# Kernel tuning notes

Hardware: AMD Instinct MI355X
Metric: run time of the kernel (lower is better)

The kernel has to match this reference:

```python
import jax, jax.numpy as jnp
import numpy as np

B, N, A = 32, 1024, 256          # batch, n_entities, n_agents
D_IN, D_H, H = 256, 256, 8       # input_dim, hidden_dim, n_heads
SCALE = 1.0 / np.sqrt(D_H)
EPS = 1e-12


def setup_inputs() -> dict:
    key = jax.random.key(0)
    ks = jax.random.split(key, 7)
    x = jax.random.normal(ks[0], (B, N, D_IN), dtype=jnp.float32)
    # binary visibility mask [batch, n_agents, n_entities]
    m = (jax.random.uniform(ks[1], (B, A, N)) > 0.5).astype(jnp.float32)
    # encoder Linear(input_dim, hidden_dim): weight [out,in], bias [out]
    W_enc = jax.random.normal(ks[2], (D_H, D_IN), dtype=jnp.float32) / np.sqrt(D_IN)
    b_enc = jnp.zeros((D_H,), dtype=jnp.float32)
    # per-head projection matrices stacked [H, D_H, D_H] (torch.randn init)
    WQ = jax.random.normal(ks[3], (H, D_H, D_H), dtype=jnp.float32)
    WK = jax.random.normal(ks[4], (H, D_H, D_H), dtype=jnp.float32)
    WV = jax.random.normal(ks[5], (H, D_H, D_H), dtype=jnp.float32)
    return {"x": x, "m": m, "W_enc": W_enc, "b_enc": b_enc, "WQ": WQ, "WK": WK, "WV": WV}


def reference(x, m, W_enc, b_enc, WQ, WK, WV):
    # encode: LeakyReLU then Linear
    h = jnp.einsum('bni,oi->bno', jax.nn.leaky_relu(x), W_enc) + b_enc  # [B,N,D_H]
    n_agents = m.shape[1]
    ha = h[:, :n_agents]                                   # [B,A,D_H]
    # per-head projections, heads vectorized
    Q = jnp.einsum('bad,hde->bhae', ha, WQ)                # [B,H,A,D_H]
    K = jnp.einsum('bnd,hde->bhne', h, WK)                 # [B,H,N,D_H]
    V = jnp.einsum('bnd,hde->bhne', h, WV)                 # [B,H,N,D_H]
    S = jnp.einsum('bhae,bhne->bhan', Q, K) * SCALE        # [B,H,A,N]
    P = jax.nn.softmax(S, axis=-1)
    P = P * m[:, None]                                     # post-softmax mask
    prob = P / (jnp.sum(P, axis=-1, keepdims=True) + EPS)  # renormalize
    z = jnp.einsum('bhan,bhne->bhae', prob, V)             # [B,H,A,D_H]
    return jnp.mean(z, axis=1)                             # [B,A,D_H]
```

## Files before the change

kernel.cpp:

```cpp
#include <hip/hip_runtime.h>
#include <math.h>

namespace {
constexpr int B_N  = 32;
constexpr int SEQ  = 1024;
constexpr int AG   = 256;
constexpr int D    = 256;
constexpr int NH   = 8;
constexpr float SCALE = 0.0625f;
constexpr float EPS   = 1e-12f;

constexpr size_t HHI_OFF  = 0;
constexpr size_t HLO_OFF  = 16777216;
constexpr size_t HT_OFF   = 33554432;
constexpr size_t MTHI_OFF = 50331648;
constexpr size_t MTLO_OFF = 51380224;
constexpr size_t MB_OFF   = 52428800;
constexpr size_t WVT_OFF  = 53477376;
constexpr size_t Z16_OFF  = 54525952;
}

typedef __attribute__((ext_vector_type(8))) short short8;
typedef __attribute__((ext_vector_type(4))) float floatx4;
#define MFMA_BF(A,B,C) __builtin_amdgcn_mfma_f32_16x16x32_bf16(A,B,C,0,0,0)

__device__ __forceinline__ unsigned short bf16_rtne(float f) {
    unsigned u = __float_as_uint(f);
    u += 0x7fffu + ((u >> 16) & 1u);
    return (unsigned short)(u >> 16);
}
__device__ __forceinline__ float bf16_tof(unsigned short h) {
    return __uint_as_float(((unsigned)h) << 16);
}
__device__ __forceinline__ void async16(void* lds, const void* g) {
    __builtin_amdgcn_global_load_lds(
        (const __attribute__((address_space(1))) unsigned int*)g,
        (__attribute__((address_space(3))) unsigned int*)lds,
        16, 0, 0);
}

__global__ __launch_bounds__(256) void enc_mfma(
    const float* __restrict__ x, const float* __restrict__ W_enc,
    const float* __restrict__ b_enc,
    ushort* __restrict__ h_hi, ushort* __restrict__ h_lo,
    ushort* __restrict__ hT)
{
    __shared__ ushort Ah[64][40], Al[64][40];
    __shared__ ushort Bh[64][40], Bl[64][40];
    __shared__ ushort Th[64][72], Tl[64][72];

    const int t    = threadIdx.x;
    const int wv   = t >> 6;
    const int lane = t & 63;
    const int l15  = lane & 15;
    const int quad = lane >> 4;
    const int col0 = blockIdx.x * 64;
    const int row0 = blockIdx.y * 64;

    floatx4 acc[4];
#pragma unroll
    for (int i = 0; i < 4; ++i) acc[i] = (floatx4){0.f, 0.f, 0.f, 0.f};

    for (int k0 = 0; k0 < 256; k0 += 32) {
        __syncthreads();
        {
            const int r = t >> 2, s = (t & 3) * 8;
            float f[8];
            *(float4*)&f[0] = *(const float4*)(x + (size_t)(row0 + r) * 256 + k0 + s);
            *(float4*)&f[4] = *(const float4*)(x + (size_t)(row0 + r) * 256 + k0 + s + 4);
            short8 hi8, lo8;
#pragma unroll
            for (int e = 0; e < 8; ++e) {
                float v = f[e] > 0.f ? f[e] : 0.01f * f[e];
                unsigned short hb = bf16_rtne(v);
                hi8[e] = (short)hb;
                lo8[e] = (short)bf16_rtne(v - bf16_tof(hb));
            }
            *(short8*)&Ah[r][s] = hi8;
            *(short8*)&Al[r][s] = lo8;
            *(float4*)&f[0] = *(const float4*)(W_enc + (size_t)(col0 + r) * 256 + k0 + s);
            *(float4*)&f[4] = *(const float4*)(W_enc + (size_t)(col0 + r) * 256 + k0 + s + 4);
#pragma unroll
            for (int e = 0; e < 8; ++e) {
                unsigned short hb = bf16_rtne(f[e]);
                hi8[e] = (short)hb;
                lo8[e] = (short)bf16_rtne(f[e] - bf16_tof(hb));
            }
            *(short8*)&Bh[r][s] = hi8;
            *(short8*)&Bl[r][s] = lo8;
        }
        __syncthreads();

        short8 Af  = *(const short8*)&Ah[wv * 16 + l15][quad * 8];
        short8 Afl = *(const short8*)&Al[wv * 16 + l15][quad * 8];
#pragma unroll
        for (int et = 0; et < 4; ++et) {
            short8 Bf  = *(const short8*)&Bh[et * 16 + l15][quad * 8];
            short8 Bfl = *(const short8*)&Bl[et * 16 + l15][quad * 8];
            acc[et] = MFMA_BF(Af,  Bf,  acc[et]);
            acc[et] = MFMA_BF(Afl, Bf,  acc[et]);
            acc[et] = MFMA_BF(Af,  Bfl, acc[et]);
        }
    }

    __syncthreads();
#pragma unroll
    for (int et = 0; et < 4; ++et) {
        const int col = et * 16 + l15;
        const float bb = b_enc[col0 + col];
#pragma unroll
        for (int r = 0; r < 4; ++r) {
            const int row = wv * 16 + quad * 4 + r;
            const float v = acc[et][r] + bb;
            const unsigned short hb = bf16_rtne(v);
            Th[row][col] = hb;
            Tl[row][col] = bf16_rtne(v - bf16_tof(hb));
        }
    }
    __syncthreads();
    {
        const int r = t >> 2, c0 = (t & 3) * 16;
        ushort* dh = h_hi + (size_t)(row0 + r) * 256 + col0 + c0;
        ushort* dl = h_lo + (size_t)(row0 + r) * 256 + col0 + c0;
        *(short8*)dh       = *(const short8*)&Th[r][c0];
        *(short8*)(dh + 8) = *(const short8*)&Th[r][c0 + 8];
        *(short8*)dl       = *(const short8*)&Tl[r][c0];
        *(short8*)(dl + 8) = *(const short8*)&Tl[r][c0 + 8];
    }
    {
        const int bq = (int)blockIdx.y >> 4;
        const int n0 = ((int)blockIdx.y & 15) * 64;
        const int dd = t >> 2, seg = (t & 3) * 16;
        ushort tmp[16];
#pragma unroll
        for (int j = 0; j < 16; ++j) tmp[j] = Th[seg + j][dd];
        ushort* dst = hT + ((size_t)(bq * 256 + col0 + dd)) * 1024 + n0 + seg;
        *(short8*)dst       = *(short8*)&tmp[0];
        *(short8*)(dst + 8) = *(short8*)&tmp[8];
    }
}

__global__ __launch_bounds__(256) void prep_fused(
    const float* __restrict__ m, unsigned* __restrict__ mb,
    const float* __restrict__ WV, ushort* __restrict__ WVt,
    const float* __restrict__ WQ, const float* __restrict__ WK,
    ushort* __restrict__ Mt_hi, ushort* __restrict__ Mt_lo)
{
    __shared__ __align__(16) char plds[17408];
    const int t = threadIdx.x;
    const int v = blockIdx.x;

    if (v < 1024) {
        const int idx = v * 256 + t;
        const float4* src = (const float4*)(m + (size_t)idx * 32);
        unsigned wbits = 0;
#pragma unroll
        for (int i = 0; i < 8; ++i) {
            float4 vv = src[i];
            wbits |= (vv.x > 0.5f ? 1u : 0u) << (i * 4 + 0);
            wbits |= (vv.y > 0.5f ? 1u : 0u) << (i * 4 + 1);
            wbits |= (vv.z > 0.5f ? 1u : 0u) << (i * 4 + 2);
            wbits |= (vv.w > 0.5f ? 1u : 0u) << (i * 4 + 3);
        }
        mb[idx] = wbits;
    } else if (v < 1152) {
        float (*T)[68] = (float(*)[68])plds;
        const int v2 = v - 1024;
        const int d0 = (v2 & 3) * 64, e0 = ((v2 >> 2) & 3) * 64, h = v2 >> 4;
        {
            const int r = t >> 2, c = (t & 3) * 16;
            const float* src = WV + ((size_t)(h * 256 + d0 + r)) * 256 + e0 + c;
#pragma unroll
            for (int j = 0; j < 4; ++j)
                *(float4*)&T[r][c + j * 4] = *(const float4*)(src + j * 4);
        }
        __syncthreads();
        {
            const int ee = t >> 2, seg = (t & 3) * 16;
            ushort tmp[16];
#pragma unroll
            for (int j = 0; j < 16; ++j) tmp[j] = bf16_rtne(T[seg + j][ee]);
            ushort* dst = WVt + ((size_t)(h * 256 + e0 + ee)) * 256 + d0 + seg;
            *(short8*)dst       = *(short8*)&tmp[0];
            *(short8*)(dst + 8) = *(short8*)&tmp[8];
        }
    } else {
        float (*AsT)[68] = (float(*)[68])plds;
        float (*BsT)[68] = (float(*)[68])(plds + 8704);
        const int v3 = v - 1152;
        const int tx = t & 15, ty = t >> 4;
        const int col0 = (v3 & 3) * 64;
        const int row0 = ((v3 >> 2) & 3) * 64;
        const int hz   = v3 >> 4;
        const float* A  = WK + (size_t)hz * 256 * 256;
        const float* Bm = WQ + (size_t)hz * 256 * 256;
        ushort* Chi = Mt_hi + (size_t)hz * 256 * 256;
        ushort* Clo = Mt_lo + (size_t)hz * 256 * 256;

        float acc[4][4];
#pragma unroll
        for (int r = 0; r < 4; ++r)
#pragma unroll
            for (int c = 0; c < 4; ++c) acc[r][c] = 0.f;

        for (int k0 = 0; k0 < 256; k0 += 32) {
            __syncthreads();
#pragma unroll
            for (int ss = 0; ss < 2; ++ss) {
                int flat = t + 256 * ss;
                int rr = flat >> 3, k4 = flat & 7;
                float4 vv = *(const float4*)(A + (size_t)(row0 + rr) * 256 + k0 + k4 * 4);
                AsT[k4*4+0][rr] = vv.x; AsT[k4*4+1][rr] = vv.y;
                AsT[k4*4+2][rr] = vv.z; AsT[k4*4+3][rr] = vv.w;
                float4 wv = *(const float4*)(Bm + (size_t)(col0 + rr) * 256 + k0 + k4 * 4);
                BsT[k4*4+0][rr] = wv.x; BsT[k4*4+1][rr] = wv.y;
                BsT[k4*4+2][rr] = wv.z; BsT[k4*4+3][rr] = wv.w;
            }
            __syncthreads();
#pragma unroll 8
            for (int kk = 0; kk < 32; ++kk) {
                float4 a4 = *(const float4*)&AsT[kk][ty * 4];
                float4 b4 = *(const float4*)&BsT[kk][tx * 4];
                const float ar[4] = {a4.x, a4.y, a4.z, a4.w};
                const float bc[4] = {b4.x, b4.y, b4.z, b4.w};
#pragma unroll
                for (int r = 0; r < 4; ++r)
#pragma unroll
                    for (int c = 0; c < 4; ++c)
                        acc[r][c] = fmaf(ar[r], bc[c], acc[r][c]);
            }
        }
#pragma unroll
        for (int r = 0; r < 4; ++r) {
            const int row = row0 + ty * 4 + r;
            ushort hi4[4], lo4[4];
#pragma unroll
            for (int c = 0; c < 4; ++c) {
                float vv = acc[r][c];
                hi4[c] = bf16_rtne(vv);
                lo4[c] = bf16_rtne(vv - bf16_tof(hi4[c]));
            }
            *(ushort4*)(Chi + (size_t)row * 256 + col0 + tx * 4) =
                make_ushort4(hi4[0], hi4[1], hi4[2], hi4[3]);
            *(ushort4*)(Clo + (size_t)row * 256 + col0 + tx * 4) =
                make_ushort4(lo4[0], lo4[1], lo4[2], lo4[3]);
        }
    }
}

__global__ __launch_bounds__(512, 2) void attn_mfma(
    const ushort* __restrict__ h_hi, const ushort* __restrict__ h_lo,
    const ushort* __restrict__ hT,   const ushort* __restrict__ Mt_hi,
    const ushort* __restrict__ Mt_lo, const unsigned* __restrict__ mbits,
    ushort* __restrict__ zout)
{
    __shared__ __align__(16) char lds[118784];
    ushort* pP = (ushort*)(lds + 98304);
    ushort* pE = (ushort*)(lds + 108544);

    const int t    = threadIdx.x;
    const int wv   = t >> 6;
    const int lane = t & 63;
    const int l15  = lane & 15;
    const int quad = lane >> 4;
    const int f    = blockIdx.x;
    const int b    = (f & 7) + 8 * (f >> 7);
    const int mid  = (f >> 3) & 15;
    const int hh   = (mid >> 2) * 2 + (wv >> 2);
    const int a0   = (mid & 3) * 64;
    const int aw   = a0 + (wv & 3) * 16;

    const ushort* hbh = h_hi + (size_t)b * SEQ * D;
    const ushort* hbl = h_lo + (size_t)b * SEQ * D;
    const ushort* hTb = hT   + (size_t)b * D * SEQ;

    floatx4 qac[16];
#pragma unroll
    for (int i = 0; i < 16; ++i) qac[i] = (floatx4){0.f, 0.f, 0.f, 0.f};

    for (int kc = 0; kc < 4; ++kc) {
        short8 Ah[2], Al[2];
#pragma unroll
        for (int kt = 0; kt < 2; ++kt) {
            const size_t ao = ((size_t)b * SEQ + aw + l15) * D +
                              kc * 64 + kt * 32 + quad * 8;
            Ah[kt] = *(const short8*)(h_hi + ao);
            Al[kt] = *(const short8*)(h_lo + ao);
        }
#pragma unroll
        for (int nt2 = 0; nt2 < 16; ++nt2) {
#pragma unroll
            for (int kt = 0; kt < 2; ++kt) {
                const size_t mo = ((size_t)hh * D + nt2 * 16 + l15) * D +
                                  kc * 64 + kt * 32 + quad * 8;
                short8 Bh = *(const short8*)(Mt_hi + mo);
                short8 Bl = *(const short8*)(Mt_lo + mo);
                qac[nt2] = MFMA_BF(Ah[kt], Bh, qac[nt2]);
                qac[nt2] = MFMA_BF(Al[kt], Bh, qac[nt2]);
                qac[nt2] = MFMA_BF(Ah[kt], Bl, qac[nt2]);
            }
        }
    }

    short8 Qhi[8], Qlo[8];
    {
        float* qscr = (float*)lds;
        for (int c = 0; c < 4; ++c) {
#pragma unroll
            for (int j = 0; j < 4; ++j)
#pragma unroll
                for (int r = 0; r < 4; ++r)
                    qscr[(wv * 16 + quad * 4 + r) * 68 + j * 16 + l15] = qac[c * 4 + j][r];
#pragma unroll
            for (int kt = 0; kt < 2; ++kt) {
                const float* pr = &qscr[(wv * 16 + l15) * 68 + kt * 32 + quad * 8];
                float ftmp[8];
                *(float4*)&ftmp[0] = *(const float4*)pr;
                *(float4*)&ftmp[4] = *(const float4*)(pr + 4);
                short8 hi, lo;
#pragma unroll
                for (int e = 0; e < 8; ++e) {
                    unsigned short hb = bf16_rtne(ftmp[e]);
                    hi[e] = (short)hb;
                    lo[e] = (short)bf16_rtne(ftmp[e] - bf16_tof(hb));
                }
                Qhi[c * 2 + kt] = hi;
                Qlo[c * 2 + kt] = lo;
            }
        }
    }
    __syncthreads();

    auto issue_tile = [&](char* buf, int n0) {
        ushort* dh = (ushort*)buf;
        ushort* dl = (ushort*)(buf + 16384);
        ushort* dT = (ushort*)(buf + 32768);
#pragma unroll
        for (int i = 0; i < 2; ++i) {
            const int slot = wv * 128 + i * 64 + lane;
            const int row  = slot >> 5;
            const int p    = slot & 31;
            const int c    = p ^ (row & 7);
            const size_t go = (size_t)(n0 + row) * 256 + c * 8;
            const size_t lo_ = (size_t)(wv * 128 + i * 64) * 8;
            async16(dh + lo_, hbh + go);
            async16(dl + lo_, hbl + go);
        }
#pragma unroll
        for (int i = 0; i < 2; ++i) {
            const int slot = wv * 128 + i * 64 + lane;
            const int row  = slot >> 2;
            const int p    = slot & 3;
            const int c    = p ^ ((row >> 2) & 3);
            async16(dT + (size_t)(wv * 128 + i * 64) * 8,
                    hTb + (size_t)row * 1024 + n0 + c * 8);
        }
    };

    issue_tile(lds,         0);
    issue_tile(lds + 49152, 32);
    __syncthreads();

    floatx4 zac[16];
#pragma unroll
    for (int i = 0; i < 16; ++i) zac[i] = (floatx4){0.f, 0.f, 0.f, 0.f};
    floatx4 zacZ = (floatx4){0.f, 0.f, 0.f, 0.f};
    floatx4 zacE = (floatx4){0.f, 0.f, 0.f, 0.f};
    float mx[4] = {-INFINITY, -INFINITY, -INFINITY, -INFINITY};

    short8 onesf;
#pragma unroll
    for (int e = 0; e < 8; ++e) onesf[e] = (short)0x3F80;

    const unsigned* mbr = mbits + ((size_t)b * AG + aw + quad * 4) * (SEQ / 32);

    for (int nt = 0; nt < 32; ++nt) {
        char* cur = lds + (size_t)(nt & 1) * 49152;
        ushort* hS_hi = (ushort*)cur;
        ushort* hS_lo = (ushort*)(cur + 16384);
        ushort* hTS   = (ushort*)(cur + 32768);

        floatx4 sacH[2], sacL[2];
        sacH[0] = (floatx4){0.f, 0.f, 0.f, 0.f};
        sacH[1] = (floatx4){0.f, 0.f, 0.f, 0.f};
        sacL[0] = (floatx4){0.f, 0.f, 0.f, 0.f};
        sacL[1] = (floatx4){0.f, 0.f, 0.f, 0.f};
#pragma unroll
        for (int ks = 0; ks < 8; ++ks) {
            const int cg = ks * 4 + quad;
#pragma unroll
            for (int ntile = 0; ntile < 2; ++ntile) {
                const int row = ntile * 16 + l15;
                const int off = row * 256 + (cg ^ (row & 7)) * 8;
                short8 Bh = *(const short8*)&hS_hi[off];
                short8 Bl = *(const short8*)&hS_lo[off];
                sacH[ntile] = MFMA_BF(Qhi[ks], Bh, sacH[ntile]);
                sacL[ntile] = MFMA_BF(Qlo[ks], Bh, sacL[ntile]);
                sacL[ntile] = MFMA_BF(Qhi[ks], Bl, sacL[ntile]);
            }
        }

        float l0[4], l1[4];
#pragma unroll
        for (int r = 0; r < 4; ++r) {
            l0[r] = (sacH[0][r] + sacL[0][r]) * SCALE;
            l1[r] = (sacH[1][r] + sacL[1][r]) * SCALE;
        }

        float mt[4];
#pragma unroll
        for (int r = 0; r < 4; ++r) mt[r] = fmaxf(l0[r], l1[r]);
#pragma unroll
        for (int off = 1; off < 16; off <<= 1) {
#pragma unroll
            for (int r = 0; r < 4; ++r)
                mt[r] = fmaxf(mt[r], __shfl_xor(mt[r], off));
        }

        const bool need = (mt[0] > mx[0] + 8.0f) || (mt[1] > mx[1] + 8.0f) ||
                          (mt[2] > mx[2] + 8.0f) || (mt[3] > mx[3] + 8.0f);
        if (__any(need)) {
            float alr[4];
#pragma unroll
            for (int r = 0; r < 4; ++r) {
                const float mxn = fmaxf(mx[r], mt[r]);
                alr[r] = __expf(mx[r] - mxn);
                mx[r] = mxn;
            }
#pragma unroll
            for (int dt = 0; dt < 16; ++dt) {
                zac[dt][0] *= alr[0]; zac[dt][1] *= alr[1];
                zac[dt][2] *= alr[2]; zac[dt][3] *= alr[3];
            }
            zacZ[0] *= alr[0]; zacZ[1] *= alr[1];
            zacZ[2] *= alr[2]; zacZ[3] *= alr[3];
            zacE[0] *= alr[0]; zacE[1] *= alr[1];
            zacE[2] *= alr[2]; zacE[3] *= alr[3];
        }

#pragma unroll
        for (int r = 0; r < 4; ++r) {
            const unsigned w0 = mbr[r * (SEQ / 32) + nt];
            const float e0 = __expf(l0[r] - mx[r]);
            const float e1 = __expf(l1[r] - mx[r]);
            const float p0 = ((w0 >> l15) & 1u)        ? e0 : 0.f;
            const float p1 = ((w0 >> (16 + l15)) & 1u) ? e1 : 0.f;
            const int row = wv * 16 + quad * 4 + r;
            pP[row * 40 + l15]      = bf16_rtne(p0);
            pP[row * 40 + 16 + l15] = bf16_rtne(p1);
            pE[row * 40 + l15]      = bf16_rtne(e0);
            pE[row * 40 + 16 + l15] = bf16_rtne(e1);
        }

        short8 Pf = *(const short8*)&pP[(wv * 16 + l15) * 40 + quad * 8];
        short8 Ef = *(const short8*)&pE[(wv * 16 + l15) * 40 + quad * 8];
        zacZ = MFMA_BF(Pf, onesf, zacZ);
        zacE = MFMA_BF(Ef, onesf, zacE);

#pragma unroll
        for (int dt = 0; dt < 16; ++dt) {
            const int row = dt * 16 + l15;
            const int p   = quad ^ ((row >> 2) & 3);
            short8 Bf = *(const short8*)&hTS[row * 32 + p * 8];
            zac[dt] = MFMA_BF(Pf, Bf, zac[dt]);
        }

        __syncthreads();
        if (nt + 2 < 32) issue_tile(cur, (nt + 2) * 32);
    }

#pragma unroll
    for (int r = 0; r < 4; ++r) {
        const int a = aw + quad * 4 + r;
        const float inv = 1.0f / (zacZ[r] + EPS * zacE[r]);
        ushort* zr = zout + (((size_t)b * NH + hh) * AG + a) * D;
#pragma unroll
        for (int dt = 0; dt < 16; ++dt)
            zr[dt * 16 + l15] = bf16_rtne(zac[dt][r] * inv);
    }
}

__global__ __launch_bounds__(256) void out_mfma(
    const ushort* __restrict__ z16, const ushort* __restrict__ WVt,
    float* __restrict__ out)
{
    const int t    = threadIdx.x;
    const int wv   = t >> 6;
    const int lane = t & 63;
    const int l15  = lane & 15;
    const int quad = lane >> 4;
    const int f    = blockIdx.x;
    const int b    = (f & 7) + 8 * (f >> 7);
    const int mid  = (f >> 3) & 15;
    const int e0   = (mid & 3) * 64;
    const int a0   = (mid >> 2) * 64;
    const int aw   = a0 + wv * 16;

    floatx4 acc[4];
#pragma unroll
    for (int i = 0; i < 4; ++i) acc[i] = (floatx4){0.f, 0.f, 0.f, 0.f};

#pragma unroll 4
    for (int c = 0; c < 64; ++c) {
        const int hh = c >> 3, d0 = (c & 7) * 32;
        short8 Af = *(const short8*)(z16 +
            (((size_t)b * NH + hh) * AG + aw + l15) * D + d0 + quad * 8);
#pragma unroll
        for (int et = 0; et < 4; ++et) {
            short8 Bf = *(const short8*)(WVt +
                ((size_t)hh * D + e0 + et * 16 + l15) * D + d0 + quad * 8);
            acc[et] = MFMA_BF(Af, Bf, acc[et]);
        }
    }
#pragma unroll
    for (int et = 0; et < 4; ++et)
#pragma unroll
        for (int r = 0; r < 4; ++r)
            out[((size_t)b * AG + aw + quad * 4 + r) * D + e0 + et * 16 + l15] =
                acc[et][r] * 0.125f;
}

extern "C" void kernel_launch(void* const* d_in, const int* in_sizes, int n_in,
                              void* d_out, int out_size, void* d_ws, size_t ws_size,
                              hipStream_t stream)
{
    (void)in_sizes; (void)n_in; (void)out_size; (void)ws_size;
    const float* x     = (const float*)d_in[0];
    const float* m     = (const float*)d_in[1];
    const float* W_enc = (const float*)d_in[2];
    const float* b_enc = (const float*)d_in[3];
    const float* WQ    = (const float*)d_in[4];
    const float* WK    = (const float*)d_in[5];
    const float* WV    = (const float*)d_in[6];
    float* out = (float*)d_out;
    char* ws = (char*)d_ws;

    ushort*   h_hi  = (ushort*)(ws + HHI_OFF);
    ushort*   h_lo  = (ushort*)(ws + HLO_OFF);
    ushort*   hT    = (ushort*)(ws + HT_OFF);
    ushort*   Mt_hi = (ushort*)(ws + MTHI_OFF);
    ushort*   Mt_lo = (ushort*)(ws + MTLO_OFF);
    unsigned* mbits = (unsigned*)(ws + MB_OFF);
    ushort*   WVt   = (ushort*)(ws + WVT_OFF);
    ushort*   z16   = (ushort*)(ws + Z16_OFF);

    enc_mfma<<<dim3(4, 512, 1), dim3(256), 0, stream>>>(
        x, W_enc, b_enc, h_hi, h_lo, hT);
    prep_fused<<<dim3(1280, 1, 1), dim3(256), 0, stream>>>(
        m, mbits, WV, WVt, WQ, WK, Mt_hi, Mt_lo);
    attn_mfma<<<dim3(512, 1, 1), dim3(512), 0, stream>>>(
        h_hi, h_lo, hT, Mt_hi, Mt_lo, mbits, z16);
    out_mfma<<<dim3(512, 1, 1), dim3(256), 0, stream>>>(z16, WVt, out);
}
```

Baseline: 527.3 us.

## Merge encoder and prep kernels into one launch; raise wave priority around MFMA loops

The encoder GEMM kernel and the mask/weight prep kernel are combined into a single launch of 3328 blocks, with blockIdx ranges dispatching to each role. This removes one kernel launch and the gap between the two, and lets the independent prep work overlap with the encoder work. s_setprio hints are also placed around the MFMA loops in the attention kernel so waves issuing matrix ops get scheduling priority. The shared LDS allocation grows to the encoder's size for every block, which may lower occupancy for the prep blocks.

```diff
diff --git a/kernel.cpp b/kernel.cpp
--- a/kernel.cpp
+++ b/kernel.cpp
@@ -39,119 +39,119 @@
         16, 0, 0);
 }
 
-__global__ __launch_bounds__(256) void enc_mfma(
+__global__ __launch_bounds__(256) void enc_prep(
     const float* __restrict__ x, const float* __restrict__ W_enc,
     const float* __restrict__ b_enc,
     ushort* __restrict__ h_hi, ushort* __restrict__ h_lo,
-    ushort* __restrict__ hT)
-{
-    __shared__ ushort Ah[64][40], Al[64][40];
-    __shared__ ushort Bh[64][40], Bl[64][40];
-    __shared__ ushort Th[64][72], Tl[64][72];
-
-    const int t    = threadIdx.x;
-    const int wv   = t >> 6;
-    const int lane = t & 63;
-    const int l15  = lane & 15;
-    const int quad = lane >> 4;
-    const int col0 = blockIdx.x * 64;
-    const int row0 = blockIdx.y * 64;
-
-    floatx4 acc[4];
-#pragma unroll
-    for (int i = 0; i < 4; ++i) acc[i] = (floatx4){0.f, 0.f, 0.f, 0.f};
-
-    for (int k0 = 0; k0 < 256; k0 += 32) {
-        __syncthreads();
-        {
-            const int r = t >> 2, s = (t & 3) * 8;
-            float f[8];
-            *(float4*)&f[0] = *(const float4*)(x + (size_t)(row0 + r) * 256 + k0 + s);
-            *(float4*)&f[4] = *(const float4*)(x + (size_t)(row0 + r) * 256 + k0 + s + 4);
-            short8 hi8, lo8;
-#pragma unroll
-            for (int e = 0; e < 8; ++e) {
-                float v = f[e] > 0.f ? f[e] : 0.01f * f[e];
-                unsigned short hb = bf16_rtne(v);
-                hi8[e] = (short)hb;
-                lo8[e] = (short)bf16_rtne(v - bf16_tof(hb));
-            }
-            *(short8*)&Ah[r][s] = hi8;
-            *(short8*)&Al[r][s] = lo8;
-            *(float4*)&f[0] = *(const float4*)(W_enc + (size_t)(col0 + r) * 256 + k0 + s);
-            *(float4*)&f[4] = *(const float4*)(W_enc + (size_t)(col0 + r) * 256 + k0 + s + 4);
-#pragma unroll
-            for (int e = 0; e < 8; ++e) {
-                unsigned short hb = bf16_rtne(f[e]);
-                hi8[e] = (short)hb;
-                lo8[e] = (short)bf16_rtne(f[e] - bf16_tof(hb));
-            }
-            *(short8*)&Bh[r][s] = hi8;
-            *(short8*)&Bl[r][s] = lo8;
-        }
-        __syncthreads();
-
-        short8 Af  = *(const short8*)&Ah[wv * 16 + l15][quad * 8];
-        short8 Afl = *(const short8*)&Al[wv * 16 + l15][quad * 8];
-#pragma unroll
-        for (int et = 0; et < 4; ++et) {
-            short8 Bf  = *(const short8*)&Bh[et * 16 + l15][quad * 8];
-            short8 Bfl = *(const short8*)&Bl[et * 16 + l15][quad * 8];
-            acc[et] = MFMA_BF(Af,  Bf,  acc[et]);
-            acc[et] = MFMA_BF(Afl, Bf,  acc[et]);
-            acc[et] = MFMA_BF(Af,  Bfl, acc[et]);
-        }
-    }
-
-    __syncthreads();
-#pragma unroll
-    for (int et = 0; et < 4; ++et) {
-        const int col = et * 16 + l15;
-        const float bb = b_enc[col0 + col];
-#pragma unroll
-        for (int r = 0; r < 4; ++r) {
-            const int row = wv * 16 + quad * 4 + r;
-            const float v = acc[et][r] + bb;
-            const unsigned short hb = bf16_rtne(v);
-            Th[row][col] = hb;
-            Tl[row][col] = bf16_rtne(v - bf16_tof(hb));
-        }
-    }
-    __syncthreads();
-    {
-        const int r = t >> 2, c0 = (t & 3) * 16;
-        ushort* dh = h_hi + (size_t)(row0 + r) * 256 + col0 + c0;
-        ushort* dl = h_lo + (size_t)(row0 + r) * 256 + col0 + c0;
-        *(short8*)dh       = *(const short8*)&Th[r][c0];
-        *(short8*)(dh + 8) = *(const short8*)&Th[r][c0 + 8];
-        *(short8*)dl       = *(const short8*)&Tl[r][c0];
-        *(short8*)(dl + 8) = *(const short8*)&Tl[r][c0 + 8];
-    }
-    {
-        const int bq = (int)blockIdx.y >> 4;
-        const int n0 = ((int)blockIdx.y & 15) * 64;
-        const int dd = t >> 2, seg = (t & 3) * 16;
-        ushort tmp[16];
-#pragma unroll
-        for (int j = 0; j < 16; ++j) tmp[j] = Th[seg + j][dd];
-        ushort* dst = hT + ((size_t)(bq * 256 + col0 + dd)) * 1024 + n0 + seg;
-        *(short8*)dst       = *(short8*)&tmp[0];
-        *(short8*)(dst + 8) = *(short8*)&tmp[8];
-    }
-}
-
-__global__ __launch_bounds__(256) void prep_fused(
+    ushort* __restrict__ hT,
     const float* __restrict__ m, unsigned* __restrict__ mb,
     const float* __restrict__ WV, ushort* __restrict__ WVt,
     const float* __restrict__ WQ, const float* __restrict__ WK,
     ushort* __restrict__ Mt_hi, ushort* __restrict__ Mt_lo)
 {
-    __shared__ __align__(16) char plds[17408];
+    __shared__ __align__(16) char slds[38912];
     const int t = threadIdx.x;
     const int v = blockIdx.x;
 
-    if (v < 1024) {
-        const int idx = v * 256 + t;
+    if (v < 2048) {
+        ushort (*Ah)[40] = (ushort(*)[40])(slds);
+        ushort (*Al)[40] = (ushort(*)[40])(slds + 5120);
+        ushort (*Bh)[40] = (ushort(*)[40])(slds + 10240);
+        ushort (*Bl)[40] = (ushort(*)[40])(slds + 15360);
+        ushort (*Th)[72] = (ushort(*)[72])(slds + 20480);
+        ushort (*Tl)[72] = (ushort(*)[72])(slds + 29696);
+
+        const int wv   = t >> 6;
+        const int lane = t & 63;
+        const int l15  = lane & 15;
+        const int quad = lane >> 4;
+        const int col0 = (v & 3) * 64;
+        const int vy   = v >> 2;
+        const int row0 = vy * 64;
+
+        floatx4 acc[4];
+#pragma unroll
+        for (int i = 0; i < 4; ++i) acc[i] = (floatx4){0.f, 0.f, 0.f, 0.f};
+
+        for (int k0 = 0; k0 < 256; k0 += 32) {
+            __syncthreads();
+            {
+                const int r = t >> 2, s = (t & 3) * 8;
+                float f[8];
+                *(float4*)&f[0] = *(const float4*)(x + (size_t)(row0 + r) * 256 + k0 + s);
+                *(float4*)&f[4] = *(const float4*)(x + (size_t)(row0 + r) * 256 + k0 + s + 4);
+                short8 hi8, lo8;
+#pragma unroll
+                for (int e = 0; e < 8; ++e) {
+                    float vv = f[e] > 0.f ? f[e] : 0.01f * f[e];
+                    unsigned short hb = bf16_rtne(vv);
+                    hi8[e] = (short)hb;
+                    lo8[e] = (short)bf16_rtne(vv - bf16_tof(hb));
+                }
+                *(short8*)&Ah[r][s] = hi8;
+                *(short8*)&Al[r][s] = lo8;
+                *(float4*)&f[0] = *(const float4*)(W_enc + (size_t)(col0 + r) * 256 + k0 + s);
+                *(float4*)&f[4] = *(const float4*)(W_enc + (size_t)(col0 + r) * 256 + k0 + s + 4);
+#pragma unroll
+                for (int e = 0; e < 8; ++e) {
+                    unsigned short hb = bf16_rtne(f[e]);
+                    hi8[e] = (short)hb;
+                    lo8[e] = (short)bf16_rtne(f[e] - bf16_tof(hb));
+                }
+                *(short8*)&Bh[r][s] = hi8;
+                *(short8*)&Bl[r][s] = lo8;
+            }
+            __syncthreads();
+
+            short8 Af  = *(const short8*)&Ah[wv * 16 + l15][quad * 8];
+            short8 Afl = *(const short8*)&Al[wv * 16 + l15][quad * 8];
+#pragma unroll
+            for (int et = 0; et < 4; ++et) {
+                short8 Bf  = *(const short8*)&Bh[et * 16 + l15][quad * 8];
+                short8 Bfl = *(const short8*)&Bl[et * 16 + l15][quad * 8];
+                acc[et] = MFMA_BF(Af,  Bf,  acc[et]);
+                acc[et] = MFMA_BF(Afl, Bf,  acc[et]);
+                acc[et] = MFMA_BF(Af,  Bfl, acc[et]);
+            }
+        }
+
+        __syncthreads();
+#pragma unroll
+        for (int et = 0; et < 4; ++et) {
+            const int col = et * 16 + l15;
+            const float bb = b_enc[col0 + col];
+#pragma unroll
+            for (int r = 0; r < 4; ++r) {
+                const int row = wv * 16 + quad * 4 + r;
+                const float vv = acc[et][r] + bb;
+                const unsigned short hb = bf16_rtne(vv);
+                Th[row][col] = hb;
+                Tl[row][col] = bf16_rtne(vv - bf16_tof(hb));
+            }
+        }
+        __syncthreads();
+        {
+            const int r = t >> 2, c0 = (t & 3) * 16;
+            ushort* dh = h_hi + (size_t)(row0 + r) * 256 + col0 + c0;
+            ushort* dl = h_lo + (size_t)(row0 + r) * 256 + col0 + c0;
+            *(short8*)dh       = *(const short8*)&Th[r][c0];
+            *(short8*)(dh + 8) = *(const short8*)&Th[r][c0 + 8];
+            *(short8*)dl       = *(const short8*)&Tl[r][c0];
+            *(short8*)(dl + 8) = *(const short8*)&Tl[r][c0 + 8];
+        }
+        {
+            const int bq = vy >> 4;
+            const int n0 = (vy & 15) * 64;
+            const int dd = t >> 2, seg = (t & 3) * 16;
+            ushort tmp[16];
+#pragma unroll
+            for (int j = 0; j < 16; ++j) tmp[j] = Th[seg + j][dd];
+            ushort* dst = hT + ((size_t)(bq * 256 + col0 + dd)) * 1024 + n0 + seg;
+            *(short8*)dst       = *(short8*)&tmp[0];
+            *(short8*)(dst + 8) = *(short8*)&tmp[8];
+        }
+    } else if (v < 3072) {
+        const int idx = (v - 2048) * 256 + t;
         const float4* src = (const float4*)(m + (size_t)idx * 32);
         unsigned wbits = 0;
 #pragma unroll
@@ -163,9 +163,9 @@
             wbits |= (vv.w > 0.5f ? 1u : 0u) << (i * 4 + 3);
         }
         mb[idx] = wbits;
-    } else if (v < 1152) {
-        float (*T)[68] = (float(*)[68])plds;
-        const int v2 = v - 1024;
+    } else if (v < 3200) {
+        float (*T)[68] = (float(*)[68])slds;
+        const int v2 = v - 3072;
         const int d0 = (v2 & 3) * 64, e0 = ((v2 >> 2) & 3) * 64, h = v2 >> 4;
         {
             const int r = t >> 2, c = (t & 3) * 16;
@@ -185,9 +185,9 @@
             *(short8*)(dst + 8) = *(short8*)&tmp[8];
         }
     } else {
-        float (*AsT)[68] = (float(*)[68])plds;
-        float (*BsT)[68] = (float(*)[68])(plds + 8704);
-        const int v3 = v - 1152;
+        float (*AsT)[68] = (float(*)[68])slds;
+        float (*BsT)[68] = (float(*)[68])(slds + 8704);
+        const int v3 = v - 3200;
         const int tx = t & 15, ty = t >> 4;
         const int col0 = (v3 & 3) * 64;
         const int row0 = ((v3 >> 2) & 3) * 64;
@@ -385,6 +385,7 @@
         sacH[1] = (floatx4){0.f, 0.f, 0.f, 0.f};
         sacL[0] = (floatx4){0.f, 0.f, 0.f, 0.f};
         sacL[1] = (floatx4){0.f, 0.f, 0.f, 0.f};
+        __builtin_amdgcn_s_setprio(1);
 #pragma unroll
         for (int ks = 0; ks < 8; ++ks) {
             const int cg = ks * 4 + quad;
@@ -399,6 +400,7 @@
                 sacL[ntile] = MFMA_BF(Qhi[ks], Bl, sacL[ntile]);
             }
         }
+        __builtin_amdgcn_s_setprio(0);
 
         float l0[4], l1[4];
 #pragma unroll
@@ -457,6 +459,7 @@
         zacZ = MFMA_BF(Pf, onesf, zacZ);
         zacE = MFMA_BF(Ef, onesf, zacE);
 
+        __builtin_amdgcn_s_setprio(1);
 #pragma unroll
         for (int dt = 0; dt < 16; ++dt) {
             const int row = dt * 16 + l15;
@@ -464,6 +467,7 @@
             short8 Bf = *(const short8*)&hTS[row * 32 + p * 8];
             zac[dt] = MFMA_BF(Pf, Bf, zac[dt]);
         }
+        __builtin_amdgcn_s_setprio(0);
 
         __syncthreads();
         if (nt + 2 < 32) issue_tile(cur, (nt + 2) * 32);
@@ -544,9 +548,8 @@
     ushort*   WVt   = (ushort*)(ws + WVT_OFF);
     ushort*   z16   = (ushort*)(ws + Z16_OFF);
 
-    enc_mfma<<<dim3(4, 512, 1), dim3(256), 0, stream>>>(
-        x, W_enc, b_enc, h_hi, h_lo, hT);
-    prep_fused<<<dim3(1280, 1, 1), dim3(256), 0, stream>>>(
+    enc_prep<<<dim3(3328, 1, 1), dim3(256), 0, stream>>>(
+        x, W_enc, b_enc, h_hi, h_lo, hT,
         m, mbits, WV, WVt, WQ, WK, Mt_hi, Mt_lo);
     attn_mfma<<<dim3(512, 1, 1), dim3(512), 0, stream>>>(
         h_hi, h_lo, hT, Mt_hi, Mt_lo, mbits, z16);
```

Result: no change. 522.8 us (-0.9%).
